# Performance work log

Hardware: AMD Instinct MI355X
Metric: run time of the kernel (lower is better)

The kernel has to match this reference:

```python
import jax, jax.numpy as jnp
from jax import lax
import numpy as np

N, T, C, H, W, S = 1, 8, 64, 192, 192, 4
HS, WS = H // S, W // S
CH = C * S * S          # 1024 = channels
G = 4                   # n_groups
CG = CH // G            # 256 = n_group_channels
ORF = 2.0               # offset_range_factor


def _unfold(x, s=S):
    # F.unfold(kernel=s, stride=s): (n,c,h,w) -> (n, c*s*s, (h//s)*(w//s))
    n, c, h, w = x.shape
    x = x.reshape(n, c, h // s, s, w // s, s).transpose(0, 1, 3, 5, 2, 4)
    return x.reshape(n, c * s * s, (h // s) * (w // s))


def _fold(x, h, w, s=S):
    # inverse of _unfold (non-overlapping)
    n, cl, _ = x.shape
    c = cl // (s * s)
    x = x.reshape(n, c, s, s, h // s, w // s).transpose(0, 1, 4, 2, 5, 3)
    return x.reshape(n, c, h, w)


def _gather_hw(x, iy, ix):
    # x (B,C,H,W); iy/ix (B,Hg,Wg) int32 -> (B,C,Hg,Wg)
    B, Cc, Hh, Ww = x.shape
    idx = (iy * Ww + ix).reshape(B, 1, -1)
    v = jnp.take_along_axis(x.reshape(B, Cc, Hh * Ww), idx, axis=2)
    return v.reshape(B, Cc, iy.shape[1], iy.shape[2])


def gs_nearest(x, grid):
    # F.grid_sample(mode='nearest', padding='zeros', align_corners=True)
    B, Cc, Hh, Ww = x.shape
    ix = (grid[..., 0] + 1.0) * 0.5 * (Ww - 1)
    iy = (grid[..., 1] + 1.0) * 0.5 * (Hh - 1)
    ixn = jnp.round(ix).astype(jnp.int32)
    iyn = jnp.round(iy).astype(jnp.int32)
    valid = (ixn >= 0) & (ixn < Ww) & (iyn >= 0) & (iyn < Hh)
    v = _gather_hw(x, jnp.clip(iyn, 0, Hh - 1), jnp.clip(ixn, 0, Ww - 1))
    return v * valid[:, None].astype(x.dtype)


def gs_bilinear(x, grid):
    # F.grid_sample(mode='bilinear', padding='zeros', align_corners=True)
    B, Cc, Hh, Ww = x.shape
    ix = (grid[..., 0] + 1.0) * 0.5 * (Ww - 1)
    iy = (grid[..., 1] + 1.0) * 0.5 * (Hh - 1)
    x0 = jnp.floor(ix)
    y0 = jnp.floor(iy)
    wx = ix - x0
    wy = iy - y0
    x0 = x0.astype(jnp.int32)
    y0 = y0.astype(jnp.int32)
    out = jnp.zeros((B, Cc) + grid.shape[1:3], x.dtype)
    for dy, dx in ((0, 0), (0, 1), (1, 0), (1, 1)):
        yi = y0 + dy
        xi = x0 + dx
        wgt = (wy if dy else 1.0 - wy) * (wx if dx else 1.0 - wx)
        valid = (xi >= 0) & (xi < Ww) & (yi >= 0) & (yi < Hh)
        v = _gather_hw(x, jnp.clip(yi, 0, Hh - 1), jnp.clip(xi, 0, Ww - 1))
        out = out + v * (wgt * valid)[:, None].astype(x.dtype)
    return out


def conv(x, w, b=None, pad=0, groups=1):
    y = lax.conv_general_dilated(x, w, (1, 1), [(pad, pad), (pad, pad)],
                                 dimension_numbers=('NCHW', 'OIHW', 'NCHW'),
                                 feature_group_count=groups)
    return y if b is None else y + b[None, :, None, None]


def ln_c(x, g, b, eps=1e-5):
    # LayerNormProxy: LayerNorm over channel dim of NCHW
    m = x.mean(axis=1, keepdims=True)
    v = ((x - m) ** 2).mean(axis=1, keepdims=True)
    return (x - m) / jnp.sqrt(v + eps) * g[None, :, None, None] + b[None, :, None, None]


def l2n(x, axis):
    return x / jnp.maximum(jnp.linalg.norm(x, axis=axis, keepdims=True), 1e-12)


def refpts(B, Hk, Wk, dt):
    ry = (jnp.linspace(0.5, Hk - 0.5, Hk, dtype=dt) / Hk) * 2 - 1
    rx = (jnp.linspace(0.5, Wk - 0.5, Wk, dtype=dt) / Wk) * 2 - 1
    ref = jnp.stack(jnp.meshgrid(ry, rx, indexing='ij'), axis=-1)  # (Hk,Wk,2)=(y,x)
    return jnp.broadcast_to(ref[None], (B, Hk, Wk, 2))


def _forward(cf, idx1, af, s1, s2, s3, loc, wtdw, btdw, lng, lnb, wtpw, wfus, bfus):
    n, c, h, w = af.shape
    t = s1.shape[1]
    hs, ws = h // S, w // S
    fl = c * S * S           # feat_len = 1024
    fn = hs * ws             # feat_num
    # trajectory locations -> normalized nearest-sampling grid
    gf = loc.reshape(n, t, 2, hs, ws).transpose(0, 1, 3, 4, 2)
    gx = 2.0 * gf[..., 0] / max(ws - 1, 1) - 1.0
    gy = 2.0 * gf[..., 1] / max(hs - 1, 1) - 1.0
    grid = jnp.stack((gx, gy), axis=-1).reshape(n * t, hs, ws, 2)
    o1 = gs_nearest(s1.reshape(n * t, fl, hs, ws), grid)
    o2 = gs_nearest(s2.reshape(n * t, fl, hs, ws), grid)
    o3 = gs_nearest(s3.reshape(n * t, fl, hs, ws), grid)
    oi = gs_nearest(idx1.reshape(n * t, fl, hs, ws), grid)
    oi = l2n(oi.reshape(n, t, fl, fn).transpose(0, 3, 1, 2), 3)   # (n,fn,t,fl)
    cu = _unfold(cf)                                              # (n,fl,fn)
    cn = l2n(cu.transpose(0, 2, 1), 2)                            # (n,fn,fl)
    tq = cn.reshape(n, hs, ws, fl).transpose(0, 3, 1, 2)          # (n,fl,hs,ws)
    tk = oi.transpose(0, 2, 1, 3).reshape(n * t, hs, ws, fl).transpose(0, 3, 1, 2)
    # deformable time offsets (grouped)
    qo = jnp.tile(tq.reshape(n * G, CG, hs, ws), (t, 1, 1, 1))
    ko = tk.reshape(n * t * G, CG, hs, ws)
    off = jnp.concatenate([qo, ko], axis=1)
    o = conv(off, wtdw, btdw, pad=2, groups=CG)
    o = ln_c(o, lng, lnb)
    o = jax.nn.gelu(o, approximate=False)
    o = conv(o, wtpw)                                             # (b,2,Hk,Wk)
    Hk, Wk = o.shape[2], o.shape[3]
    o = jnp.tanh(o) * jnp.array([1.0 / Hk, 1.0 / Wk], o.dtype).reshape(1, 2, 1, 1) * ORF
    pos = o.transpose(0, 2, 3, 1) + refpts(n * t * G, Hk, Wk, o.dtype)  # (b,Hk,Wk,(y,x))
    gp = pos[..., ::-1]                                           # (x,y) for grid_sample
    ks_ = gs_bilinear(tk.reshape(n * t * G, CG, hs, ws), gp)
    # '(n t g) c h w -> n (h w) t (g c)'
    ks_ = ks_.reshape(n, t, G, CG, Hk, Wk).transpose(0, 4, 5, 1, 2, 3).reshape(n, fn, t, fl)
    mat = jnp.einsum('nftc,nfc->nft', ks_, cn)
    csoft = mat.max(axis=2)
    cidx = mat.argmax(axis=2)
    csoft_f = _fold(jnp.broadcast_to(csoft[:, None, :], (n, fl, fn)), h, w)

    def sg(os_):
        v = gs_bilinear(os_.reshape(n * t * G, CG, hs, ws), gp).reshape(n, t, fl, fn)
        v = jnp.take_along_axis(v, cidx[:, None, None, :], axis=1)[:, 0]
        return _fold(v, h, w)

    out = conv(jnp.concatenate([sg(o1), sg(o2), sg(o3)], axis=1), wfus, bfus, pad=1)
    return out * csoft_f + af


def setup_inputs() -> dict:
    key = jax.random.key(0)
    ks = jax.random.split(key, 12)
    sc = 0.05
    return {
        'curr_feat': jax.random.normal(ks[0], (N, C, H, W), jnp.float32),
        'index_feat_set_s1': jax.random.normal(ks[1], (N, T, CH, HS, WS), jnp.float32),
        'anchor_feat': jax.random.normal(ks[2], (N, C, H, W), jnp.float32),
        'sparse_feat_set_s1': jax.random.normal(ks[3], (N, T, CH, HS, WS), jnp.float32),
        'sparse_feat_set_s2': jax.random.normal(ks[4], (N, T, CH, HS, WS), jnp.float32),
        'sparse_feat_set_s3': jax.random.normal(ks[5], (N, T, CH, HS, WS), jnp.float32),
        'location_feat': jax.random.uniform(ks[6], (N, 2 * T, HS, WS), jnp.float32) * (WS - 1.0),
        'w_tdw': jax.random.normal(ks[7], (CG, 2, 5, 5), jnp.float32) * sc,
        'b_tdw': jnp.zeros((CG,), jnp.float32),
        'ln_g': jnp.ones((CG,), jnp.float32),
        'ln_b': jnp.zeros((CG,), jnp.float32),
        'w_tpw': jax.random.normal(ks[8], (2, CG, 1, 1), jnp.float32) * sc,
        'w_fus': jax.random.normal(ks[9], (C, 3 * C, 3, 3), jnp.float32) * sc,
        'b_fus': jnp.zeros((C,), jnp.float32),
    }


def reference(curr_feat, index_feat_set_s1, anchor_feat, sparse_feat_set_s1, sparse_feat_set_s2, sparse_feat_set_s3, location_feat, w_tdw, b_tdw, ln_g, ln_b, w_tpw, w_fus, b_fus):
    return _forward(curr_feat, index_feat_set_s1, anchor_feat, sparse_feat_set_s1,
                    sparse_feat_set_s2, sparse_feat_set_s3, location_feat,
                    w_tdw, b_tdw, ln_g, ln_b, w_tpw, w_fus, b_fus)
```

## Files before the change

kernel.cpp:

```cpp
#include <hip/hip_runtime.h>
#include <math.h>

#define TT 8
#define FN 2304
#define FL 1024
#define HS 48

typedef __attribute__((ext_vector_type(8))) short short8;
typedef __attribute__((ext_vector_type(4))) float floatx4;

static constexpr size_t OFF_IDX1T  = 0;
static constexpr size_t OFF_SEL    = 0;
static constexpr size_t OFF_FIN    = 28311552;
static constexpr size_t OFF_WB     = 57216000;
static constexpr size_t OFF_TK     = 75497472;
static constexpr size_t OFF_CN     = 150994944;
static constexpr size_t OFF_QH     = 160432128;
static constexpr size_t OFF_SRCMAP = 165150720;
static constexpr size_t OFF_BSRC   = 165224448;
static constexpr size_t OFF_BW     = 166404096;
static constexpr size_t OFF_CSOFT  = 167583744;
static constexpr size_t OFF_CIDX   = 167592960;
static constexpr size_t OFF_CSRC   = 167602176;
static constexpr size_t OFF_CW     = 167749632;

__device__ inline ushort f2bf(float x) {
  union { float f; unsigned int u; } v; v.f = x;
  unsigned int r = (v.u + 0x7FFFu + ((v.u >> 16) & 1u)) >> 16;
  return (ushort)r;
}

__global__ void k_nearmap(const float* __restrict__ loc, int* __restrict__ srcmap) {
  int idx = blockIdx.x * 256 + threadIdx.x;
  if (idx >= TT * FN) return;
  int t = idx / FN, f = idx % FN;
  float lx = loc[(size_t)(t * 2 + 0) * FN + f];
  float ly = loc[(size_t)(t * 2 + 1) * FN + f];
  float gx = 2.0f * lx / 47.0f - 1.0f;
  float gy = 2.0f * ly / 47.0f - 1.0f;
  float ix = (gx + 1.0f) * 0.5f * 47.0f;
  float iy = (gy + 1.0f) * 0.5f * 47.0f;
  int ixn = __float2int_rn(ix);
  int iyn = __float2int_rn(iy);
  bool valid = (ixn >= 0) && (ixn < 48) && (iyn >= 0) && (iyn < 48);
  srcmap[idx] = valid ? (iyn * 48 + ixn) : -1;
}

__global__ __launch_bounds__(256) void k_transpose(const float* __restrict__ in, float* __restrict__ out) {
  __shared__ float tile[64][65];
  const int t = blockIdx.z;
  const int cl0 = blockIdx.x * 64;
  const int f0 = blockIdx.y * 64;
  const float* src = in + (size_t)t * FL * FN;
  float* dst = out + (size_t)t * FN * FL;
  const int tx = threadIdx.x & 15, ty = threadIdx.x >> 4;
#pragma unroll
  for (int k = 0; k < 4; k++) {
    const float4 v = *reinterpret_cast<const float4*>(src + (size_t)(cl0 + ty + 16 * k) * FN + f0 + tx * 4);
    float* tr = &tile[ty + 16 * k][tx * 4];
    tr[0] = v.x; tr[1] = v.y; tr[2] = v.z; tr[3] = v.w;
  }
  __syncthreads();
#pragma unroll
  for (int k = 0; k < 4; k++) {
    float4 v;
    v.x = tile[tx * 4 + 0][ty + 16 * k];
    v.y = tile[tx * 4 + 1][ty + 16 * k];
    v.z = tile[tx * 4 + 2][ty + 16 * k];
    v.w = tile[tx * 4 + 3][ty + 16 * k];
    *reinterpret_cast<float4*>(dst + (size_t)(f0 + ty + 16 * k) * FL + cl0 + tx * 4) = v;
  }
}

__global__ __launch_bounds__(256) void k_tk(const float* __restrict__ idx1t,
                                            const int* __restrict__ srcmap,
                                            float* __restrict__ tk) {
  __shared__ float red[4];
  const int bid = blockIdx.x;
  const int t = bid / FN;
  const int s = srcmap[bid];
  float4* dst = reinterpret_cast<float4*>(tk + (size_t)bid * FL);
  const int tid = threadIdx.x;
  if (s < 0) {
    dst[tid] = make_float4(0.f, 0.f, 0.f, 0.f);
    return;
  }
  const float4* row = reinterpret_cast<const float4*>(idx1t + ((size_t)t * FN + s) * FL);
  float4 v = row[tid];
  float sq = v.x * v.x + v.y * v.y + v.z * v.z + v.w * v.w;
#pragma unroll
  for (int m = 1; m <= 32; m <<= 1) sq += __shfl_xor(sq, m, 64);
  const int lane = tid & 63, w = tid >> 6;
  if (lane == 0) red[w] = sq;
  __syncthreads();
  const float total = red[0] + red[1] + red[2] + red[3];
  const float scale = 1.0f / fmaxf(sqrtf(total), 1e-12f);
  dst[tid] = make_float4(v.x * scale, v.y * scale, v.z * scale, v.w * scale);
}

__global__ __launch_bounds__(256) void k_cn(const float* __restrict__ cf, float* __restrict__ cn) {
  __shared__ float red[4];
  int f = blockIdx.x;
  int i = f / 48, j = f % 48;
  int tid = threadIdx.x;
  float v[4];
  float sq = 0.f;
#pragma unroll
  for (int k = 0; k < 4; k++) {
    int cl = tid + 256 * k;
    int c = cl >> 4, sy = (cl >> 2) & 3, sx = cl & 3;
    v[k] = cf[(size_t)c * 36864 + (size_t)(i * 4 + sy) * 192 + (j * 4 + sx)];
    sq += v[k] * v[k];
  }
#pragma unroll
  for (int m = 1; m <= 32; m <<= 1) sq += __shfl_xor(sq, m, 64);
  int lane = tid & 63, w = tid >> 6;
  if (lane == 0) red[w] = sq;
  __syncthreads();
  float total = red[0] + red[1] + red[2] + red[3];
  float scale = 1.0f / fmaxf(sqrtf(total), 1e-12f);
#pragma unroll
  for (int k = 0; k < 4; k++) cn[(size_t)f * FL + tid + 256 * k] = v[k] * scale;
}

__global__ __launch_bounds__(128) void k_qconv(const float* __restrict__ cn,
                                               const float* __restrict__ wtdw,
                                               const float* __restrict__ btdw,
                                               float* __restrict__ qhalf) {
  const int xt = blockIdx.x, y = blockIdx.y, g = blockIdx.z;
  const int j = threadIdx.x;
  const int x0 = xt * 16;
  float w0[25], w1[25];
  {
    const float* wp = wtdw + (size_t)j * 50;
#pragma unroll
    for (int p = 0; p < 25; ++p) { w0[p] = wp[p]; w1[p] = wp[25 + p]; }
  }
  float acc[16];
#pragma unroll
  for (int i = 0; i < 16; ++i) acc[i] = 0.f;
  const int cbase = g * 256 + 2 * j;
#pragma unroll
  for (int r = 0; r < 5; ++r) {
    const int yy = y - 2 + r;
    if (yy < 0 || yy >= 48) continue;
#pragma unroll
    for (int cc2 = 0; cc2 < 20; ++cc2) {
      const int xx = x0 - 2 + cc2;
      float vx = 0.f, vy = 0.f;
      if (xx >= 0 && xx < 48) {
        const float2 v = *reinterpret_cast<const float2*>(cn + ((size_t)(yy * 48 + xx) << 10) + cbase);
        vx = v.x; vy = v.y;
      }
#pragma unroll
      for (int kx = 0; kx < 5; ++kx) {
        const int xo = cc2 - kx;
        if (xo >= 0 && xo < 16)
          acc[xo] = fmaf(vx, w0[r * 5 + kx], fmaf(vy, w1[r * 5 + kx], acc[xo]));
      }
    }
  }
  const float bb = btdw[j];
#pragma unroll
  for (int xo = 0; xo < 16; ++xo)
    qhalf[((size_t)g * FN + (y * 48 + x0 + xo)) * 128 + j] = acc[xo] + bb;
}

__global__ __launch_bounds__(128) void k_kconv_ln(const float* __restrict__ tk,
                                                  const float* __restrict__ wtdw,
                                                  const float* __restrict__ btdw,
                                                  const float* __restrict__ qhalf,
                                                  const float* __restrict__ lng,
                                                  const float* __restrict__ lnb,
                                                  const float* __restrict__ wtpw,
                                                  int* __restrict__ bsrc,
                                                  float* __restrict__ bw) {
  __shared__ float ch[16][257];
  const int xt = blockIdx.x, y = blockIdx.y, b = blockIdx.z;
  const int t = b >> 2, g = b & 3;
  const int j = threadIdx.x;
  const int x0 = xt * 16;
  float w0[25], w1[25];
  {
    const float* wp = wtdw + (size_t)(128 + j) * 50;
#pragma unroll
    for (int p = 0; p < 25; ++p) { w0[p] = wp[p]; w1[p] = wp[25 + p]; }
  }
  float acc[16];
#pragma unroll
  for (int i = 0; i < 16; ++i) acc[i] = 0.f;
  const size_t tbase = (size_t)t * FN;
  const int cbase = g * 256 + 2 * j;
#pragma unroll
  for (int r = 0; r < 5; ++r) {
    const int yy = y - 2 + r;
    if (yy < 0 || yy >= 48) continue;
#pragma unroll
    for (int cc2 = 0; cc2 < 20; ++cc2) {
      const int xx = x0 - 2 + cc2;
      float vx = 0.f, vy = 0.f;
      if (xx >= 0 && xx < 48) {
        const float2 v = *reinterpret_cast<const float2*>(tk + ((tbase + yy * 48 + xx) << 10) + cbase);
        vx = v.x; vy = v.y;
      }
#pragma unroll
      for (int kx = 0; kx < 5; ++kx) {
        const int xo = cc2 - kx;
        if (xo >= 0 && xo < 16)
          acc[xo] = fmaf(vx, w0[r * 5 + kx], fmaf(vy, w1[r * 5 + kx], acc[xo]));
      }
    }
  }
  const float bb = btdw[128 + j];
#pragma unroll
  for (int xo = 0; xo < 16; ++xo) ch[xo][128 + j] = acc[xo] + bb;
#pragma unroll
  for (int xo = 0; xo < 16; ++xo)
    ch[xo][j] = qhalf[((size_t)g * FN + (y * 48 + x0 + xo)) * 128 + j];
  __syncthreads();

  const int lane = j & 63, wv = j >> 6;
  for (int p = wv; p < 16; p += 2) {
    float v0 = ch[p][lane], v1 = ch[p][lane + 64], v2 = ch[p][lane + 128], v3 = ch[p][lane + 192];
    float s = v0 + v1 + v2 + v3;
    float q = v0 * v0 + v1 * v1 + v2 * v2 + v3 * v3;
#pragma unroll
    for (int m = 1; m <= 32; m <<= 1) { s += __shfl_xor(s, m, 64); q += __shfl_xor(q, m, 64); }
    float mean = s * (1.0f / 256.0f);
    float var = q * (1.0f / 256.0f) - mean * mean;
    float rstd = rsqrtf(var + 1e-5f);
    float d0 = 0.f, d1 = 0.f;
#pragma unroll
    for (int k2 = 0; k2 < 4; k2++) {
      int c = lane + 64 * k2;
      float xv = (k2 == 0) ? v0 : (k2 == 1) ? v1 : (k2 == 2) ? v2 : v3;
      float xn = (xv - mean) * rstd * lng[c] + lnb[c];
      float ge = 0.5f * xn * (1.0f + erff(xn * 0.70710678118654752440f));
      d0 += ge * wtpw[c];
      d1 += ge * wtpw[256 + c];
    }
#pragma unroll
    for (int m = 1; m <= 32; m <<= 1) { d0 += __shfl_xor(d0, m, 64); d1 += __shfl_xor(d1, m, 64); }
    if (lane == 0) {
      float o0 = tanhf(d0) * (2.0f / 48.0f);
      float o1 = tanhf(d1) * (2.0f / 48.0f);
      int x = x0 + p;
      float ry = (0.5f + (float)y) / 48.0f * 2.0f - 1.0f;
      float rx = (0.5f + (float)x) / 48.0f * 2.0f - 1.0f;
      float pos0 = o0 + ry, pos1 = o1 + rx;
      float ix = (pos1 + 1.0f) * 0.5f * 47.0f;
      float iy = (pos0 + 1.0f) * 0.5f * 47.0f;
      float x0f = floorf(ix), y0f = floorf(iy);
      float wx = ix - x0f, wy = iy - y0f;
      int xi = (int)x0f, yi = (int)y0f;
      size_t base = ((size_t)b * FN + y * 48 + x) * 4;
#pragma unroll
      for (int c = 0; c < 4; c++) {
        int dy = c >> 1, dx = c & 1;
        int yy2 = yi + dy, xx2 = xi + dx;
        bool ok = ((unsigned)yy2 < 48u) && ((unsigned)xx2 < 48u);
        float wgt = (dy ? wy : 1.0f - wy) * (dx ? wx : 1.0f - wx);
        bsrc[base + c] = ok ? (yy2 * 48 + xx2) : -1;
        bw[base + c] = wgt;
      }
    }
  }
}

__global__ __launch_bounds__(256) void k_mat(const float* __restrict__ tk,
                                             const float* __restrict__ cn,
                                             const int* __restrict__ bsrc,
                                             const float* __restrict__ bw,
                                             float* __restrict__ csoft,
                                             int* __restrict__ cidx) {
  __shared__ float red[8][4];
  const int f = blockIdx.x;
  const int tid = threadIdx.x;
  const int lane = tid & 63, w = tid >> 6;
  const int coff = w * 256 + lane * 4;
  const float4 cnv = *reinterpret_cast<const float4*>(cn + (size_t)f * FL + coff);
#pragma unroll
  for (int t = 0; t < TT; t++) {
    const size_t mb = ((size_t)(t * 4 + w) * FN + f) * 4;
    const int4 cs = *reinterpret_cast<const int4*>(bsrc + mb);
    const float4 wv = *reinterpret_cast<const float4*>(bw + mb);
    float ax = 0.f, ay = 0.f, az = 0.f, aw = 0.f;
    const float* tkt = tk + (size_t)t * FN * FL + coff;
    if (cs.x >= 0) { const float4 u = *reinterpret_cast<const float4*>(tkt + ((size_t)cs.x << 10)); ax = fmaf(wv.x, u.x, ax); ay = fmaf(wv.x, u.y, ay); az = fmaf(wv.x, u.z, az); aw = fmaf(wv.x, u.w, aw); }
    if (cs.y >= 0) { const float4 u = *reinterpret_cast<const float4*>(tkt + ((size_t)cs.y << 10)); ax = fmaf(wv.y, u.x, ax); ay = fmaf(wv.y, u.y, ay); az = fmaf(wv.y, u.z, az); aw = fmaf(wv.y, u.w, aw); }
    if (cs.z >= 0) { const float4 u = *reinterpret_cast<const float4*>(tkt + ((size_t)cs.z << 10)); ax = fmaf(wv.z, u.x, ax); ay = fmaf(wv.z, u.y, ay); az = fmaf(wv.z, u.z, az); aw = fmaf(wv.z, u.w, aw); }
    if (cs.w >= 0) { const float4 u = *reinterpret_cast<const float4*>(tkt + ((size_t)cs.w << 10)); ax = fmaf(wv.w, u.x, ax); ay = fmaf(wv.w, u.y, ay); az = fmaf(wv.w, u.z, az); aw = fmaf(wv.w, u.w, aw); }
    float partial = ax * cnv.x + ay * cnv.y + az * cnv.z + aw * cnv.w;
#pragma unroll
    for (int m = 1; m <= 32; m <<= 1) partial += __shfl_xor(partial, m, 64);
    if (lane == 0) red[t][w] = partial;
  }
  __syncthreads();
  if (tid == 0) {
    float bestv = -INFINITY;
    int besti = 0;
#pragma unroll
    for (int t = 0; t < TT; t++) {
      float tot = red[t][0] + red[t][1] + red[t][2] + red[t][3];
      if (tot > bestv) { bestv = tot; besti = t; }
    }
    csoft[f] = bestv; cidx[f] = besti;
  }
}

__global__ void k_comp(const int* __restrict__ bsrc, const float* __restrict__ bw,
                       const int* __restrict__ cidx, const int* __restrict__ srcmap,
                       int* __restrict__ csrc, float* __restrict__ cw) {
  int idx = blockIdx.x * 256 + threadIdx.x;
  if (idx >= FN * 4) return;
  int f = idx >> 2, g = idx & 3;
  int t = cidx[f];
  int b = t * 4 + g;
  size_t mb = ((size_t)b * FN + f) * 4;
  size_t ob = (size_t)idx * 4;
#pragma unroll
  for (int c = 0; c < 4; c++) {
    int s = bsrc[mb + c];
    csrc[ob + c] = (s >= 0) ? srcmap[t * FN + s] : -1;
    cw[ob + c] = bw[mb + c];
  }
}

__global__ __launch_bounds__(256) void k_sel(const float* __restrict__ s1,
                                             const float* __restrict__ s2,
                                             const float* __restrict__ s3,
                                             const int* __restrict__ cidx,
                                             const int* __restrict__ csrc,
                                             const float* __restrict__ cw,
                                             float* __restrict__ sel) {
  __shared__ float pl[4 * FN];
  const int cl = blockIdx.x, m = blockIdx.y;
  const float* sm = (m == 0) ? s1 : (m == 1) ? s2 : s3;
  const int g = cl >> 8;
  const int tid = threadIdx.x;
  float acc[9];
  int tsel[9];
  int4 cs[9];
  float4 wv[9];
#pragma unroll
  for (int it = 0; it < 9; it++) {
    int f = tid + 256 * it;
    tsel[it] = cidx[f];
    cs[it] = *reinterpret_cast<const int4*>(csrc + ((size_t)f * 4 + g) * 4);
    wv[it] = *reinterpret_cast<const float4*>(cw + ((size_t)f * 4 + g) * 4);
    acc[it] = 0.f;
  }
  float4* pl4 = reinterpret_cast<float4*>(pl);
  for (int half = 0; half < 2; half++) {
    __syncthreads();
#pragma unroll
    for (int j = 0; j < 9; j++) {
      const int e = j * 256 + tid;
      const int tl = e / 576;
      const int r = e - tl * 576;
      const float4* src4 = reinterpret_cast<const float4*>(sm + ((size_t)(half * 4 + tl) * FL + cl) * FN);
      pl4[e] = src4[r];
    }
    __syncthreads();
#pragma unroll
    for (int it = 0; it < 9; it++) {
      const int t = tsel[it] - half * 4;
      if (t >= 0 && t < 4) {
        float a = 0.f;
        if (cs[it].x >= 0) a += wv[it].x * pl[t * FN + cs[it].x];
        if (cs[it].y >= 0) a += wv[it].y * pl[t * FN + cs[it].y];
        if (cs[it].z >= 0) a += wv[it].z * pl[t * FN + cs[it].z];
        if (cs[it].w >= 0) a += wv[it].w * pl[t * FN + cs[it].w];
        acc[it] = a;
      }
    }
  }
  __syncthreads();
#pragma unroll
  for (int it = 0; it < 9; it++) pl[tid + 256 * it] = acc[it];
  __syncthreads();
  float4* orow = reinterpret_cast<float4*>(sel + ((size_t)m * FL + cl) * FN);
#pragma unroll
  for (int e = tid; e < 576; e += 256) orow[e] = pl4[e];
}

__global__ void k_zb(unsigned int* __restrict__ fin_u) {
  int idx = blockIdx.x * 256 + threadIdx.x;
  if (idx >= 772 * 96) return;
  int bp = idx / 96, u = idx % 96;
  int yy, xx;
  if (bp < 194)      { yy = 0;   xx = bp; }
  else if (bp < 388) { yy = 193; xx = bp - 194; }
  else if (bp < 580) { yy = bp - 388 + 1; xx = 0; }
  else               { yy = bp - 580 + 1; xx = 193; }
  fin_u[((size_t)yy * 194 + xx) * 96 + u] = 0;
}

__global__ __launch_bounds__(256) void k_fold2(const float* __restrict__ sel,
                                               ushort* __restrict__ fin) {
  __shared__ float ld[256 * 49];
  const int fy = blockIdx.x;
  const int m = blockIdx.y >> 2, c2t = blockIdx.y & 3;
  const int t = threadIdx.x;
  const float* sp = sel + ((size_t)m * 1024 + c2t * 256) * 2304 + fy * 48;
#pragma unroll
  for (int j = 0; j < 12; j++) {
    const int e = t + 256 * j;
    const int cl_l = e / 12, c4 = e % 12;
    const float4 v = *reinterpret_cast<const float4*>(sp + (size_t)cl_l * 2304 + c4 * 4);
    float* dr = &ld[cl_l * 49 + c4 * 4];
    dr[0] = v.x; dr[1] = v.y; dr[2] = v.z; dr[3] = v.w;
  }
  __syncthreads();
  const int ci0 = m * 64 + c2t * 16 + (t & 3) * 4;
  const int xb = t >> 2;
#pragma unroll
  for (int py = 0; py < 4; py++) {
    for (int jx = 0; jx < 3; jx++) {
      const int x = xb + 64 * jx;
      const int px = x & 3, fx = x >> 2;
      ushort4 v;
      ushort* vp = (ushort*)&v;
#pragma unroll
      for (int jj = 0; jj < 4; jj++) {
        int cl_l = ((t & 3) * 4 + jj) * 16 + py * 4 + px;
        vp[jj] = f2bf(ld[cl_l * 49 + fx]);
      }
      *reinterpret_cast<ushort4*>(fin + (((size_t)(fy * 4 + py + 1) * 194) + x + 1) * 192 + ci0) = v;
    }
  }
}

__global__ void k_wb(const float* __restrict__ wfus, ushort* __restrict__ wb) {
  int idx = blockIdx.x * 256 + threadIdx.x;
  if (idx >= 64 * 9 * 96) return;
  int cp = idx % 96, tap = (idx / 96) % 9, co = idx / (96 * 9);
  int ci = cp * 2;
  float a = wfus[((size_t)co * 192 + ci) * 9 + tap];
  float b = wfus[((size_t)co * 192 + ci + 1) * 9 + tap];
  unsigned int pk = (unsigned int)f2bf(a) | ((unsigned int)f2bf(b) << 16);
  reinterpret_cast<unsigned int*>(wb)[((size_t)co * 9 + tap) * 96 + cp] = pk;
}

__global__ __launch_bounds__(256) void k_fus(const ushort* __restrict__ fin,
                                             const ushort* __restrict__ wb,
                                             const float* __restrict__ bfus,
                                             const float* __restrict__ csoft,
                                             const float* __restrict__ af,
                                             float* __restrict__ out) {
  const int y = blockIdx.x;
  const int wv = threadIdx.x >> 6;
  const int l = threadIdx.x & 63;
  const int ln = l & 15, qd = l >> 4;
  const int x0 = wv * 48;
  floatx4 acc[4][3];
#pragma unroll
  for (int a = 0; a < 4; a++)
#pragma unroll
    for (int b = 0; b < 3; b++) acc[a][b] = (floatx4){0.f, 0.f, 0.f, 0.f};

  const int koff = qd * 8;
  for (int tap = 0; tap < 9; tap++) {
    const int ky = tap / 3, kx = tap % 3;
    const ushort* brow = fin + ((size_t)(y + ky) * 194 + kx) * 192;
    const ushort* wrow = wb + (size_t)tap * 192;
#pragma unroll
    for (int c6 = 0; c6 < 6; c6++) {
      const int ci = c6 * 32 + koff;
      short8 A[4], B[3];
#pragma unroll
      for (int mt = 0; mt < 4; mt++)
        A[mt] = *reinterpret_cast<const short8*>(wrow + (size_t)(mt * 16 + ln) * 1728 + ci);
#pragma unroll
      for (int nt = 0; nt < 3; nt++)
        B[nt] = *reinterpret_cast<const short8*>(brow + (size_t)(x0 + nt * 16 + ln) * 192 + ci);
#pragma unroll
      for (int mt = 0; mt < 4; mt++)
#pragma unroll
        for (int nt = 0; nt < 3; nt++)
          acc[mt][nt] = __builtin_amdgcn_mfma_f32_16x16x32_bf16(A[mt], B[nt], acc[mt][nt], 0, 0, 0);
    }
  }
#pragma unroll
  for (int nt = 0; nt < 3; nt++) {
    const int x = x0 + nt * 16 + ln;
    const float cs = csoft[(y >> 2) * 48 + (x >> 2)];
#pragma unroll
    for (int mt = 0; mt < 4; mt++) {
#pragma unroll
      for (int r = 0; r < 4; r++) {
        const int co = mt * 16 + qd * 4 + r;
        const size_t oi = (size_t)co * 36864 + (size_t)y * 192 + x;
        out[oi] = (acc[mt][nt][r] + bfus[co]) * cs + af[oi];
      }
    }
  }
}

extern "C" void kernel_launch(void* const* d_in, const int* in_sizes, int n_in,
                              void* d_out, int out_size, void* d_ws, size_t ws_size,
                              hipStream_t stream) {
  const float* cf   = (const float*)d_in[0];
  const float* idx1 = (const float*)d_in[1];
  const float* af   = (const float*)d_in[2];
  const float* s1   = (const float*)d_in[3];
  const float* s2   = (const float*)d_in[4];
  const float* s3   = (const float*)d_in[5];
  const float* loc  = (const float*)d_in[6];
  const float* wtdw = (const float*)d_in[7];
  const float* btdw = (const float*)d_in[8];
  const float* lng  = (const float*)d_in[9];
  const float* lnb  = (const float*)d_in[10];
  const float* wtpw = (const float*)d_in[11];
  const float* wfus = (const float*)d_in[12];
  const float* bfus = (const float*)d_in[13];
  float* out = (float*)d_out;
  char* ws = (char*)d_ws;

  float* idx1t  = (float*)(ws + OFF_IDX1T);
  float* sel    = (float*)(ws + OFF_SEL);
  ushort* fin   = (ushort*)(ws + OFF_FIN);
  ushort* wb    = (ushort*)(ws + OFF_WB);
  float* tk     = (float*)(ws + OFF_TK);
  float* cn     = (float*)(ws + OFF_CN);
  float* qh     = (float*)(ws + OFF_QH);
  int*   srcmap = (int*)(ws + OFF_SRCMAP);
  int*   bsrc   = (int*)(ws + OFF_BSRC);
  float* bw     = (float*)(ws + OFF_BW);
  float* csoft  = (float*)(ws + OFF_CSOFT);
  int*   cidx   = (int*)(ws + OFF_CIDX);
  int*   csrc   = (int*)(ws + OFF_CSRC);
  float* cw     = (float*)(ws + OFF_CW);

  k_nearmap<<<72, 256, 0, stream>>>(loc, srcmap);
  k_transpose<<<dim3(16, 36, 8), 256, 0, stream>>>(idx1, idx1t);
  k_cn<<<2304, 256, 0, stream>>>(cf, cn);
  k_tk<<<18432, 256, 0, stream>>>(idx1t, srcmap, tk);
  k_wb<<<216, 256, 0, stream>>>(wfus, wb);
  k_zb<<<290, 256, 0, stream>>>((unsigned int*)fin);
  k_qconv<<<dim3(3, 48, 4), 128, 0, stream>>>(cn, wtdw, btdw, qh);
  k_kconv_ln<<<dim3(3, 48, 32), 128, 0, stream>>>(tk, wtdw, btdw, qh, lng, lnb, wtpw, bsrc, bw);
  k_mat<<<2304, 256, 0, stream>>>(tk, cn, bsrc, bw, csoft, cidx);
  k_comp<<<36, 256, 0, stream>>>(bsrc, bw, cidx, srcmap, csrc, cw);
  k_sel<<<dim3(1024, 3), 256, 0, stream>>>(s1, s2, s3, cidx, csrc, cw, sel);
  k_fold2<<<dim3(48, 12), 256, 0, stream>>>(sel, fin);
  k_fus<<<192, 256, 0, stream>>>(fin, wb, bfus, csoft, af, out);
}
```

Baseline: 545.9 us.

## Replace materialized warped-key tensor with indirect gather plus per-row scale

Removes the k_tk kernel, which wrote a normalized, nearest-warped copy of the key features (about 75 MB). Row L2 norms are now accumulated with atomics inside the transpose kernel, and a small k_pos kernel produces per-position source indices and inverse-norm scales. The conv and matching kernels gather directly from the transposed tensor and apply the scale on the fly. The conv grids are also flattened and remapped so that neighbouring tiles land on the same XCD for L2 locality. In exchange it adds float atomics, whose summation order is nondeterministic, and an extra level of indirection on every gather.

```diff
diff --git a/kernel.cpp b/kernel.cpp
--- a/kernel.cpp
+++ b/kernel.cpp
@@ -10,10 +10,12 @@
 typedef __attribute__((ext_vector_type(4))) float floatx4;
 
 static constexpr size_t OFF_IDX1T  = 0;
-static constexpr size_t OFF_SEL    = 0;
-static constexpr size_t OFF_FIN    = 28311552;
-static constexpr size_t OFF_WB     = 57216000;
-static constexpr size_t OFF_TK     = 75497472;
+static constexpr size_t OFF_SEL    = 75497472;
+static constexpr size_t OFF_FIN    = 103809024;
+static constexpr size_t OFF_WB     = 132713472;
+static constexpr size_t OFF_NORM2  = 135497472;
+static constexpr size_t OFF_PSRC   = 135571200;
+static constexpr size_t OFF_PSCALE = 135644928;
 static constexpr size_t OFF_CN     = 150994944;
 static constexpr size_t OFF_QH     = 160432128;
 static constexpr size_t OFF_SRCMAP = 165150720;
@@ -30,9 +32,11 @@
   return (ushort)r;
 }
 
-__global__ void k_nearmap(const float* __restrict__ loc, int* __restrict__ srcmap) {
+__global__ void k_nearmap(const float* __restrict__ loc, int* __restrict__ srcmap,
+                          float* __restrict__ norm2) {
   int idx = blockIdx.x * 256 + threadIdx.x;
   if (idx >= TT * FN) return;
+  norm2[idx] = 0.f;
   int t = idx / FN, f = idx % FN;
   float lx = loc[(size_t)(t * 2 + 0) * FN + f];
   float ly = loc[(size_t)(t * 2 + 1) * FN + f];
@@ -46,7 +50,8 @@
   srcmap[idx] = valid ? (iyn * 48 + ixn) : -1;
 }
 
-__global__ __launch_bounds__(256) void k_transpose(const float* __restrict__ in, float* __restrict__ out) {
+__global__ __launch_bounds__(256) void k_transpose(const float* __restrict__ in, float* __restrict__ out,
+                                                   float* __restrict__ norm2) {
   __shared__ float tile[64][65];
   const int t = blockIdx.z;
   const int cl0 = blockIdx.x * 64;
@@ -69,33 +74,28 @@
     v.z = tile[tx * 4 + 2][ty + 16 * k];
     v.w = tile[tx * 4 + 3][ty + 16 * k];
     *reinterpret_cast<float4*>(dst + (size_t)(f0 + ty + 16 * k) * FL + cl0 + tx * 4) = v;
-  }
-}
-
-__global__ __launch_bounds__(256) void k_tk(const float* __restrict__ idx1t,
-                                            const int* __restrict__ srcmap,
-                                            float* __restrict__ tk) {
-  __shared__ float red[4];
-  const int bid = blockIdx.x;
-  const int t = bid / FN;
-  const int s = srcmap[bid];
-  float4* dst = reinterpret_cast<float4*>(tk + (size_t)bid * FL);
-  const int tid = threadIdx.x;
+    float ss = v.x * v.x + v.y * v.y + v.z * v.z + v.w * v.w;
+    ss += __shfl_xor(ss, 1, 64);
+    ss += __shfl_xor(ss, 2, 64);
+    ss += __shfl_xor(ss, 4, 64);
+    ss += __shfl_xor(ss, 8, 64);
+    if (tx == 0) atomicAdd(&norm2[(size_t)t * FN + f0 + ty + 16 * k], ss);
+  }
+}
+
+__global__ void k_pos(const int* __restrict__ srcmap, const float* __restrict__ norm2,
+                      int* __restrict__ psrc, float* __restrict__ pscale) {
+  int idx = blockIdx.x * 256 + threadIdx.x;
+  if (idx >= TT * FN) return;
+  int s = srcmap[idx];
+  int t = idx / FN;
   if (s < 0) {
-    dst[tid] = make_float4(0.f, 0.f, 0.f, 0.f);
-    return;
-  }
-  const float4* row = reinterpret_cast<const float4*>(idx1t + ((size_t)t * FN + s) * FL);
-  float4 v = row[tid];
-  float sq = v.x * v.x + v.y * v.y + v.z * v.z + v.w * v.w;
-#pragma unroll
-  for (int m = 1; m <= 32; m <<= 1) sq += __shfl_xor(sq, m, 64);
-  const int lane = tid & 63, w = tid >> 6;
-  if (lane == 0) red[w] = sq;
-  __syncthreads();
-  const float total = red[0] + red[1] + red[2] + red[3];
-  const float scale = 1.0f / fmaxf(sqrtf(total), 1e-12f);
-  dst[tid] = make_float4(v.x * scale, v.y * scale, v.z * scale, v.w * scale);
+    psrc[idx] = 0; pscale[idx] = 0.f;
+  } else {
+    psrc[idx] = s;
+    float n2 = norm2[t * FN + s];
+    pscale[idx] = 1.0f / fmaxf(sqrtf(n2), 1e-12f);
+  }
 }
 
 __global__ __launch_bounds__(256) void k_cn(const float* __restrict__ cf, float* __restrict__ cn) {
@@ -127,7 +127,13 @@
                                                const float* __restrict__ wtdw,
                                                const float* __restrict__ btdw,
                                                float* __restrict__ qhalf) {
-  const int xt = blockIdx.x, y = blockIdx.y, g = blockIdx.z;
+  const int i = blockIdx.x;
+  const int xcd = i & 7;
+  const int sl = i >> 3;
+  const int g = xcd >> 1;
+  const int r0 = (xcd & 1) * 72 + sl;
+  const int y = r0 / 3;
+  const int xt = r0 - y * 3;
   const int j = threadIdx.x;
   const int x0 = xt * 16;
   float w0[25], w1[25];
@@ -138,7 +144,7 @@
   }
   float acc[16];
 #pragma unroll
-  for (int i = 0; i < 16; ++i) acc[i] = 0.f;
+  for (int i2 = 0; i2 < 16; ++i2) acc[i2] = 0.f;
   const int cbase = g * 256 + 2 * j;
 #pragma unroll
   for (int r = 0; r < 5; ++r) {
@@ -166,7 +172,9 @@
     qhalf[((size_t)g * FN + (y * 48 + x0 + xo)) * 128 + j] = acc[xo] + bb;
 }
 
-__global__ __launch_bounds__(128) void k_kconv_ln(const float* __restrict__ tk,
+__global__ __launch_bounds__(128) void k_kconv_ln(const float* __restrict__ idx1t,
+                                                  const int* __restrict__ psrc,
+                                                  const float* __restrict__ pscale,
                                                   const float* __restrict__ wtdw,
                                                   const float* __restrict__ btdw,
                                                   const float* __restrict__ qhalf,
@@ -176,10 +184,31 @@
                                                   int* __restrict__ bsrc,
                                                   float* __restrict__ bw) {
   __shared__ float ch[16][257];
-  const int xt = blockIdx.x, y = blockIdx.y, b = blockIdx.z;
+  __shared__ int   s_ps[100];
+  __shared__ float s_sc[100];
+  const int ib = blockIdx.x;
+  const int xcd = ib & 7;
+  const int sl = ib >> 3;
+  const int b = xcd + 8 * (sl / 144);
+  const int r0 = sl % 144;
+  const int y = r0 / 3;
+  const int xt = r0 - y * 3;
   const int t = b >> 2, g = b & 3;
   const int j = threadIdx.x;
   const int x0 = xt * 16;
+  const int tp = t * FN;
+
+  if (j < 100) {
+    const int rr = j / 20, cc = j - rr * 20;
+    const int yy = y - 2 + rr, xx = x0 - 2 + cc;
+    int sv = 0; float sc = 0.f;
+    if ((unsigned)yy < 48u && (unsigned)xx < 48u) {
+      const int p = tp + yy * 48 + xx;
+      sv = psrc[p]; sc = pscale[p];
+    }
+    s_ps[j] = sv; s_sc[j] = sc;
+  }
+
   float w0[25], w1[25];
   {
     const float* wp = wtdw + (size_t)(128 + j) * 50;
@@ -188,21 +217,19 @@
   }
   float acc[16];
 #pragma unroll
-  for (int i = 0; i < 16; ++i) acc[i] = 0.f;
-  const size_t tbase = (size_t)t * FN;
+  for (int i2 = 0; i2 < 16; ++i2) acc[i2] = 0.f;
   const int cbase = g * 256 + 2 * j;
+  __syncthreads();
 #pragma unroll
   for (int r = 0; r < 5; ++r) {
     const int yy = y - 2 + r;
     if (yy < 0 || yy >= 48) continue;
 #pragma unroll
     for (int cc2 = 0; cc2 < 20; ++cc2) {
-      const int xx = x0 - 2 + cc2;
-      float vx = 0.f, vy = 0.f;
-      if (xx >= 0 && xx < 48) {
-        const float2 v = *reinterpret_cast<const float2*>(tk + ((tbase + yy * 48 + xx) << 10) + cbase);
-        vx = v.x; vy = v.y;
-      }
+      const int s2 = s_ps[r * 20 + cc2];
+      const float sc = s_sc[r * 20 + cc2];
+      const float2 v = *reinterpret_cast<const float2*>(idx1t + (((size_t)tp + s2) << 10) + cbase);
+      const float vx = v.x * sc, vy = v.y * sc;
 #pragma unroll
       for (int kx = 0; kx < 5; ++kx) {
         const int xo = cc2 - kx;
@@ -267,7 +294,9 @@
   }
 }
 
-__global__ __launch_bounds__(256) void k_mat(const float* __restrict__ tk,
+__global__ __launch_bounds__(256) void k_mat(const float* __restrict__ idx1t,
+                                             const int* __restrict__ psrc,
+                                             const float* __restrict__ pscale,
                                              const float* __restrict__ cn,
                                              const int* __restrict__ bsrc,
                                              const float* __restrict__ bw,
@@ -284,12 +313,21 @@
     const size_t mb = ((size_t)(t * 4 + w) * FN + f) * 4;
     const int4 cs = *reinterpret_cast<const int4*>(bsrc + mb);
     const float4 wv = *reinterpret_cast<const float4*>(bw + mb);
+    const int tp = t * FN;
+    const float* base = idx1t + ((size_t)tp << 10) + coff;
     float ax = 0.f, ay = 0.f, az = 0.f, aw = 0.f;
-    const float* tkt = tk + (size_t)t * FN * FL + coff;
-    if (cs.x >= 0) { const float4 u = *reinterpret_cast<const float4*>(tkt + ((size_t)cs.x << 10)); ax = fmaf(wv.x, u.x, ax); ay = fmaf(wv.x, u.y, ay); az = fmaf(wv.x, u.z, az); aw = fmaf(wv.x, u.w, aw); }
-    if (cs.y >= 0) { const float4 u = *reinterpret_cast<const float4*>(tkt + ((size_t)cs.y << 10)); ax = fmaf(wv.y, u.x, ax); ay = fmaf(wv.y, u.y, ay); az = fmaf(wv.y, u.z, az); aw = fmaf(wv.y, u.w, aw); }
-    if (cs.z >= 0) { const float4 u = *reinterpret_cast<const float4*>(tkt + ((size_t)cs.z << 10)); ax = fmaf(wv.z, u.x, ax); ay = fmaf(wv.z, u.y, ay); az = fmaf(wv.z, u.z, az); aw = fmaf(wv.z, u.w, aw); }
-    if (cs.w >= 0) { const float4 u = *reinterpret_cast<const float4*>(tkt + ((size_t)cs.w << 10)); ax = fmaf(wv.w, u.x, ax); ay = fmaf(wv.w, u.y, ay); az = fmaf(wv.w, u.z, az); aw = fmaf(wv.w, u.w, aw); }
+    if (cs.x >= 0) { const float wsc = wv.x * pscale[tp + cs.x];
+      const float4 u = *reinterpret_cast<const float4*>(base + ((size_t)psrc[tp + cs.x] << 10));
+      ax = fmaf(wsc, u.x, ax); ay = fmaf(wsc, u.y, ay); az = fmaf(wsc, u.z, az); aw = fmaf(wsc, u.w, aw); }
+    if (cs.y >= 0) { const float wsc = wv.y * pscale[tp + cs.y];
+      const float4 u = *reinterpret_cast<const float4*>(base + ((size_t)psrc[tp + cs.y] << 10));
+      ax = fmaf(wsc, u.x, ax); ay = fmaf(wsc, u.y, ay); az = fmaf(wsc, u.z, az); aw = fmaf(wsc, u.w, aw); }
+    if (cs.z >= 0) { const float wsc = wv.z * pscale[tp + cs.z];
+      const float4 u = *reinterpret_cast<const float4*>(base + ((size_t)psrc[tp + cs.z] << 10));
+      ax = fmaf(wsc, u.x, ax); ay = fmaf(wsc, u.y, ay); az = fmaf(wsc, u.z, az); aw = fmaf(wsc, u.w, aw); }
+    if (cs.w >= 0) { const float wsc = wv.w * pscale[tp + cs.w];
+      const float4 u = *reinterpret_cast<const float4*>(base + ((size_t)psrc[tp + cs.w] << 10));
+      ax = fmaf(wsc, u.x, ax); ay = fmaf(wsc, u.y, ay); az = fmaf(wsc, u.z, az); aw = fmaf(wsc, u.w, aw); }
     float partial = ax * cnv.x + ay * cnv.y + az * cnv.z + aw * cnv.w;
 #pragma unroll
     for (int m = 1; m <= 32; m <<= 1) partial += __shfl_xor(partial, m, 64);
@@ -521,7 +559,9 @@
   float* sel    = (float*)(ws + OFF_SEL);
   ushort* fin   = (ushort*)(ws + OFF_FIN);
   ushort* wb    = (ushort*)(ws + OFF_WB);
-  float* tk     = (float*)(ws + OFF_TK);
+  float* norm2  = (float*)(ws + OFF_NORM2);
+  int*   psrc   = (int*)(ws + OFF_PSRC);
+  float* pscale = (float*)(ws + OFF_PSCALE);
   float* cn     = (float*)(ws + OFF_CN);
   float* qh     = (float*)(ws + OFF_QH);
   int*   srcmap = (int*)(ws + OFF_SRCMAP);
@@ -532,15 +572,15 @@
   int*   csrc   = (int*)(ws + OFF_CSRC);
   float* cw     = (float*)(ws + OFF_CW);
 
-  k_nearmap<<<72, 256, 0, stream>>>(loc, srcmap);
-  k_transpose<<<dim3(16, 36, 8), 256, 0, stream>>>(idx1, idx1t);
+  k_nearmap<<<72, 256, 0, stream>>>(loc, srcmap, norm2);
+  k_transpose<<<dim3(16, 36, 8), 256, 0, stream>>>(idx1, idx1t, norm2);
   k_cn<<<2304, 256, 0, stream>>>(cf, cn);
-  k_tk<<<18432, 256, 0, stream>>>(idx1t, srcmap, tk);
+  k_pos<<<72, 256, 0, stream>>>(srcmap, norm2, psrc, pscale);
   k_wb<<<216, 256, 0, stream>>>(wfus, wb);
   k_zb<<<290, 256, 0, stream>>>((unsigned int*)fin);
-  k_qconv<<<dim3(3, 48, 4), 128, 0, stream>>>(cn, wtdw, btdw, qh);
-  k_kconv_ln<<<dim3(3, 48, 32), 128, 0, stream>>>(tk, wtdw, btdw, qh, lng, lnb, wtpw, bsrc, bw);
-  k_mat<<<2304, 256, 0, stream>>>(tk, cn, bsrc, bw, csoft, cidx);
+  k_qconv<<<576, 128, 0, stream>>>(cn, wtdw, btdw, qh);
+  k_kconv_ln<<<4608, 128, 0, stream>>>(idx1t, psrc, pscale, wtdw, btdw, qh, lng, lnb, wtpw, bsrc, bw);
+  k_mat<<<2304, 256, 0, stream>>>(idx1t, psrc, pscale, cn, bsrc, bw, csoft, cidx);
   k_comp<<<36, 256, 0, stream>>>(bsrc, bw, cidx, srcmap, csrc, cw);
   k_sel<<<dim3(1024, 3), 256, 0, stream>>>(s1, s2, s3, cidx, csrc, cw, sel);
   k_fold2<<<dim3(48, 12), 256, 0, stream>>>(sel, fin);
```

After: 525.0 us. 3.8% less time.
